# Performance work log

Measured on AMD Instinct MI355X. Metric: run time of the kernel, lower is better.

## Reference

```python
import jax, jax.numpy as jnp
import numpy as np

BATCH, LENGTH, IN, STATE, OUT = 8, 4096, 512, 256, 512


def setup_inputs() -> dict:
    key = jax.random.key(0)
    k1, k2, k3, k4, k5 = jax.random.split(key, 5)
    u = jax.random.normal(k1, (BATCH, LENGTH, IN), dtype=jnp.float32)
    x0 = jax.random.normal(k2, (BATCH, STATE), dtype=jnp.float32)
    A = 0.9999 * (2.0 * jax.random.uniform(k3, (STATE,), dtype=jnp.float32) - 1.0)
    B = jax.random.normal(k4, (IN, STATE), dtype=jnp.float32) / (STATE + IN) ** 0.5
    C = jax.random.normal(k5, (STATE, OUT), dtype=jnp.float32) / STATE ** 0.5
    return {"u": u, "x0": x0, "A": A, "B": B, "C": C}


def reference(u, x0, A, B, C):
    L = u.shape[1]
    # A_powers[t, n] = A[n] ** t, shape [L, state]
    A_powers = jnp.power(A[None, :], jnp.arange(L, dtype=u.dtype)[:, None])
    uB = u @ B  # [batch, L, state]
    # FFT convolution; inputs are real so rfft/irfft gives same result as
    # real(ifft(fft*fft)) in the original.
    T = 2 ** int(np.ceil(np.log2(2 * L - 1)))
    Af = jnp.fft.rfft(A_powers, n=T, axis=0)  # [T/2+1, state]
    Uf = jnp.fft.rfft(uB, n=T, axis=1)        # [batch, T/2+1, state]
    x = jnp.fft.irfft(Af[None, :, :] * Uf, n=T, axis=1)[:, :L]  # [batch, L, state]
    # initial-state contribution: A * A_powers * x0
    x = x + A[None, None, :] * A_powers[None, :, :] * x0[:, None, :]
    y = x @ C  # [batch, L, out]
    return (y, x[:, -1])
```

## Files before the change

### kernel.cpp

```cpp
#include <hip/hip_runtime.h>

#define BATCH   8
#define LENGTH  4096
#define IN_DIM  512
#define STATE   256
#define OUT_DIM 512
#define NC      64
#define LC      64

typedef __attribute__((ext_vector_type(8))) short bf16x8;
typedef __attribute__((ext_vector_type(4))) float f32x4;

union FragU { bf16x8 v; unsigned u[4]; };

__device__ __forceinline__ unsigned short bf16_rne(float v) {
    unsigned u = __builtin_bit_cast(unsigned, v);
    unsigned r = (u + 0x7FFFu + ((u >> 16) & 1u)) >> 16;
    return (unsigned short)r;
}
__device__ __forceinline__ float bf16_f(unsigned short h) {
    unsigned u = ((unsigned)h) << 16;
    return __builtin_bit_cast(float, u);
}

__global__ __launch_bounds__(256) void split_T_kernel(
    const float* __restrict__ in, unsigned short* __restrict__ hi,
    unsigned short* __restrict__ lo, int kbits, int Nsrc)
{
    int id = blockIdx.x * 256 + threadIdx.x;
    int k = id & ((1 << kbits) - 1);
    int n = id >> kbits;
    float v = in[(size_t)k * Nsrc + n];
    unsigned short h = bf16_rne(v);
    hi[id] = h;
    lo[id] = bf16_rne(v - bf16_f(h));
}

__global__ __launch_bounds__(512, 4) void gemm_dbuf(
    const float* __restrict__ Af, const unsigned short* __restrict__ Bthi,
    const unsigned short* __restrict__ Btlo, float* __restrict__ Cc,
    int N_, int K)
{
    __shared__ unsigned short lds[2 * 16384];

    const int tid  = threadIdx.x;
    const int wave = tid >> 6;
    const int lane = tid & 63;
    const int n0 = blockIdx.x * 128;
    const int m0 = blockIdx.y * 128;

    const char* gp[4];
    int ldsoff[4], gstep[4];
    #pragma unroll
    for (int t = 0; t < 4; ++t) {
        int gi = wave * 4 + t;
        if (gi < 16) {
            int p = gi * 64 + lane;
            int row = p >> 3, s = p & 7;
            int l = s ^ (row & 7);
            gp[t] = (const char*)(Af + (size_t)(m0 + row) * K + l * 4);
            gstep[t] = 32 * 4;
            ldsoff[t] = gi * 512;
        } else {
            int q2 = (gi - 16) >> 3;
            int pi = gi & 7;
            int p = pi * 64 + lane;
            int row = p >> 2, s = p & 3;
            int l = s ^ ((row >> 1) & 3);
            const unsigned short* base = q2 ? Btlo : Bthi;
            gp[t] = (const char*)(base + (size_t)(n0 + row) * K + l * 8);
            gstep[t] = 32 * 2;
            ldsoff[t] = 8192 + q2 * 4096 + pi * 512;
        }
    }

    const int r = lane & 15, q = lane >> 4;
    const int wm = (wave >> 2) * 64, wn = (wave & 3) * 32;

    int aoff[4][2], boff[2];
    #pragma unroll
    for (int i = 0; i < 4; ++i) {
        int row = wm + i * 16 + r;
        #pragma unroll
        for (int h = 0; h < 2; ++h)
            aoff[i][h] = row * 64 + ((2 * q + h) ^ (row & 7)) * 8;
    }
    #pragma unroll
    for (int j = 0; j < 2; ++j) {
        int row = wn + j * 16 + r;
        boff[j] = row * 32 + (q ^ ((row >> 1) & 3)) * 8;
    }

    f32x4 acc[4][2];
    #pragma unroll
    for (int i = 0; i < 4; ++i)
        #pragma unroll
        for (int j = 0; j < 2; ++j)
            acc[i][j] = (f32x4){0.f, 0.f, 0.f, 0.f};

    #pragma unroll
    for (int t = 0; t < 4; ++t) {
        __builtin_amdgcn_global_load_lds(
            (const __attribute__((address_space(1))) unsigned*)(gp[t]),
            (__attribute__((address_space(3))) unsigned*)(&lds[ldsoff[t]]),
            16, 0, 0);
        gp[t] += gstep[t];
    }

    const int nit = K >> 5;
    for (int it = 0; it < nit; ++it) {
        asm volatile("" ::: "memory");
        __builtin_amdgcn_s_barrier();
        asm volatile("" ::: "memory");
        if (it + 1 < nit) {
            const int bb = ((it + 1) & 1) * 16384;
            #pragma unroll
            for (int t = 0; t < 4; ++t) {
                __builtin_amdgcn_global_load_lds(
                    (const __attribute__((address_space(1))) unsigned*)(gp[t]),
                    (__attribute__((address_space(3))) unsigned*)(&lds[bb + ldsoff[t]]),
                    16, 0, 0);
                gp[t] += gstep[t];
            }
            __builtin_amdgcn_s_waitcnt(0x0F74);
        } else {
            __builtin_amdgcn_s_waitcnt(0x0F70);
        }
        asm volatile("" ::: "memory");
        __builtin_amdgcn_s_barrier();
        asm volatile("" ::: "memory");

        const unsigned short* buf = &lds[(it & 1) * 16384];

        FragU ahi[4], alo[4];
        #pragma unroll
        for (int i = 0; i < 4; ++i) {
            #pragma unroll
            for (int h = 0; h < 2; ++h) {
                float4 f = *(const float4*)(buf + aoff[i][h]);
                unsigned bx = __builtin_bit_cast(unsigned, f.x);
                unsigned by = __builtin_bit_cast(unsigned, f.y);
                unsigned bz = __builtin_bit_cast(unsigned, f.z);
                unsigned bw = __builtin_bit_cast(unsigned, f.w);
                ahi[i].u[h * 2]     = __builtin_amdgcn_perm(by, bx, 0x07060302);
                ahi[i].u[h * 2 + 1] = __builtin_amdgcn_perm(bw, bz, 0x07060302);
                float lx = f.x - __builtin_bit_cast(float, bx & 0xFFFF0000u);
                float ly = f.y - __builtin_bit_cast(float, by & 0xFFFF0000u);
                float lz = f.z - __builtin_bit_cast(float, bz & 0xFFFF0000u);
                float lw = f.w - __builtin_bit_cast(float, bw & 0xFFFF0000u);
                alo[i].u[h * 2]     = __builtin_amdgcn_perm(
                    __builtin_bit_cast(unsigned, ly), __builtin_bit_cast(unsigned, lx), 0x07060302);
                alo[i].u[h * 2 + 1] = __builtin_amdgcn_perm(
                    __builtin_bit_cast(unsigned, lw), __builtin_bit_cast(unsigned, lz), 0x07060302);
            }
        }
        FragU bhi[2], blo[2];
        #pragma unroll
        for (int j = 0; j < 2; ++j) {
            bhi[j].v = *(const bf16x8*)(buf +  8192 + boff[j]);
            blo[j].v = *(const bf16x8*)(buf + 12288 + boff[j]);
        }
        #pragma unroll
        for (int i = 0; i < 4; ++i)
            #pragma unroll
            for (int j = 0; j < 2; ++j) {
                acc[i][j] = __builtin_amdgcn_mfma_f32_16x16x32_bf16(ahi[i].v, bhi[j].v, acc[i][j], 0, 0, 0);
                acc[i][j] = __builtin_amdgcn_mfma_f32_16x16x32_bf16(alo[i].v, bhi[j].v, acc[i][j], 0, 0, 0);
                acc[i][j] = __builtin_amdgcn_mfma_f32_16x16x32_bf16(ahi[i].v, blo[j].v, acc[i][j], 0, 0, 0);
            }
    }

    #pragma unroll
    for (int i = 0; i < 4; ++i) {
        #pragma unroll
        for (int reg = 0; reg < 4; ++reg) {
            int mg = m0 + wm + i * 16 + q * 4 + reg;
            float* dst = Cc + (size_t)mg * N_ + n0 + wn + r;
            dst[0]  = acc[i][0][reg];
            dst[16] = acc[i][1][reg];
        }
    }
}

__global__ __launch_bounds__(256) void scan_carry(
    const float* __restrict__ uB, const float* __restrict__ A,
    float* __restrict__ carry)
{
    const int b = blockIdx.x;
    const int c = blockIdx.y;
    const int n = threadIdx.x;
    const float a = A[n];
    const float* p = uB + ((size_t)b * LENGTH + (size_t)c * LC) * STATE + n;
    float s = 0.f;
    #pragma unroll 8
    for (int j = 0; j < LC; ++j) s = a * s + p[(size_t)j * STATE];
    carry[((size_t)b * NC + c) * STATE + n] = s;
}

__global__ __launch_bounds__(256) void scan_apply(
    const float* __restrict__ uB, const float* __restrict__ A,
    const float* __restrict__ carry, const float* __restrict__ x0,
    float* __restrict__ x, float* __restrict__ x_last)
{
    const int b = blockIdx.x;
    const int c = blockIdx.y;
    const int n = threadIdx.x;
    const float a = A[n];
    float a2 = a * a, a4 = a2 * a2, a8 = a4 * a4, a16 = a8 * a8, a32 = a16 * a16;
    const float aLC = a32 * a32;

    float s = x0[(size_t)b * STATE + n];
    for (int d = 0; d < c; ++d)
        s = aLC * s + carry[((size_t)b * NC + d) * STATE + n];

    const size_t base = ((size_t)b * LENGTH + (size_t)c * LC) * STATE + n;
    const float* p = uB + base;
    float* qx = x + base;
    #pragma unroll 8
    for (int j = 0; j < LC; ++j) {
        s = a * s + p[(size_t)j * STATE];
        qx[(size_t)j * STATE] = s;
    }
    if (c == NC - 1) x_last[(size_t)b * STATE + n] = s;
}

extern "C" void kernel_launch(void* const* d_in, const int* in_sizes, int n_in,
                              void* d_out, int out_size, void* d_ws, size_t ws_size,
                              hipStream_t stream)
{
    const float* u  = (const float*)d_in[0];
    const float* x0 = (const float*)d_in[1];
    const float* A  = (const float*)d_in[2];
    const float* B  = (const float*)d_in[3];
    const float* C  = (const float*)d_in[4];

    const size_t MB = 1024 * 1024;
    char* ws = (char*)d_ws;

    float* x     = (float*)(ws);
    float* carry = (float*)(ws + 32 * MB);
    unsigned short* Bt_hi = (unsigned short*)(ws + 33 * MB);
    unsigned short* Bt_lo = (unsigned short*)(ws + 33 * MB + 256 * 1024);
    unsigned short* Ct_hi = (unsigned short*)(ws + 33 * MB + 512 * 1024);
    unsigned short* Ct_lo = (unsigned short*)(ws + 33 * MB + 768 * 1024);

    float* y      = (float*)d_out;
    float* x_last = y + (size_t)BATCH * LENGTH * OUT_DIM;
    float* uB     = (float*)((char*)d_out + 32 * MB);

    const int M = BATCH * LENGTH;

    split_T_kernel<<<dim3((IN_DIM * STATE) / 256), dim3(256), 0, stream>>>(B, Bt_hi, Bt_lo, 9, STATE);
    split_T_kernel<<<dim3((STATE * OUT_DIM) / 256), dim3(256), 0, stream>>>(C, Ct_hi, Ct_lo, 8, OUT_DIM);

    gemm_dbuf<<<dim3(STATE / 128, M / 128), dim3(512), 0, stream>>>(
        u, Bt_hi, Bt_lo, uB, STATE, IN_DIM);

    scan_carry<<<dim3(BATCH, NC), dim3(256), 0, stream>>>(uB, A, carry);
    scan_apply<<<dim3(BATCH, NC), dim3(256), 0, stream>>>(uB, A, carry, x0, x, x_last);

    gemm_dbuf<<<dim3(OUT_DIM / 128, M / 128), dim3(512), 0, stream>>>(
        x, Ct_hi, Ct_lo, y, OUT_DIM, STATE);
}
```

Baseline: 207.7 us.

## Emit bf16 hi/lo planes from scan and add presplit GEMM for output projection

The scan now writes the state as two bf16 planes (hi and lo) instead of fp32. A new GEMM kernel loads those pre-split planes straight into LDS, so the second GEMM skips the per-iteration fp32 split work. The two weight-split kernels are merged into one launch, and the first GEMM's wave tiling changes from 64x32 to 32x64 per wave. The lo plane comes from truncating the residual rather than rounding it, which slightly changes numerics.

```diff
diff --git a/kernel.cpp b/kernel.cpp
--- a/kernel.cpp
+++ b/kernel.cpp
@@ -23,17 +23,26 @@
     return __builtin_bit_cast(float, u);
 }
 
-__global__ __launch_bounds__(256) void split_T_kernel(
-    const float* __restrict__ in, unsigned short* __restrict__ hi,
-    unsigned short* __restrict__ lo, int kbits, int Nsrc)
+__global__ __launch_bounds__(256) void split_weights(
+    const float* __restrict__ B, const float* __restrict__ C,
+    unsigned short* __restrict__ Bhi, unsigned short* __restrict__ Blo,
+    unsigned short* __restrict__ Chi, unsigned short* __restrict__ Clo)
 {
     int id = blockIdx.x * 256 + threadIdx.x;
-    int k = id & ((1 << kbits) - 1);
-    int n = id >> kbits;
-    float v = in[(size_t)k * Nsrc + n];
-    unsigned short h = bf16_rne(v);
-    hi[id] = h;
-    lo[id] = bf16_rne(v - bf16_f(h));
+    if (id < IN_DIM * STATE) {
+        int k = id & (IN_DIM - 1), n = id >> 9;
+        float v = B[(size_t)k * STATE + n];
+        unsigned short h = bf16_rne(v);
+        Bhi[id] = h;
+        Blo[id] = bf16_rne(v - bf16_f(h));
+    } else {
+        int id2 = id - IN_DIM * STATE;
+        int k = id2 & (STATE - 1), n = id2 >> 8;
+        float v = C[(size_t)k * OUT_DIM + n];
+        unsigned short h = bf16_rne(v);
+        Chi[id2] = h;
+        Clo[id2] = bf16_rne(v - bf16_f(h));
+    }
 }
 
 __global__ __launch_bounds__(512, 4) void gemm_dbuf(
@@ -75,27 +84,27 @@
     }
 
     const int r = lane & 15, q = lane >> 4;
-    const int wm = (wave >> 2) * 64, wn = (wave & 3) * 32;
-
-    int aoff[4][2], boff[2];
-    #pragma unroll
-    for (int i = 0; i < 4; ++i) {
+    const int wm = (wave >> 1) * 32, wn = (wave & 1) * 64;
+
+    int aoff[2][2], boff[4];
+    #pragma unroll
+    for (int i = 0; i < 2; ++i) {
         int row = wm + i * 16 + r;
         #pragma unroll
         for (int h = 0; h < 2; ++h)
             aoff[i][h] = row * 64 + ((2 * q + h) ^ (row & 7)) * 8;
     }
     #pragma unroll
-    for (int j = 0; j < 2; ++j) {
+    for (int j = 0; j < 4; ++j) {
         int row = wn + j * 16 + r;
         boff[j] = row * 32 + (q ^ ((row >> 1) & 3)) * 8;
     }
 
-    f32x4 acc[4][2];
-    #pragma unroll
-    for (int i = 0; i < 4; ++i)
-        #pragma unroll
-        for (int j = 0; j < 2; ++j)
+    f32x4 acc[2][4];
+    #pragma unroll
+    for (int i = 0; i < 2; ++i)
+        #pragma unroll
+        for (int j = 0; j < 4; ++j)
             acc[i][j] = (f32x4){0.f, 0.f, 0.f, 0.f};
 
     #pragma unroll
@@ -132,9 +141,9 @@
 
         const unsigned short* buf = &lds[(it & 1) * 16384];
 
-        FragU ahi[4], alo[4];
-        #pragma unroll
-        for (int i = 0; i < 4; ++i) {
+        FragU ahi[2], alo[2];
+        #pragma unroll
+        for (int i = 0; i < 2; ++i) {
             #pragma unroll
             for (int h = 0; h < 2; ++h) {
                 float4 f = *(const float4*)(buf + aoff[i][h]);
@@ -154,6 +163,128 @@
                     __builtin_bit_cast(unsigned, lw), __builtin_bit_cast(unsigned, lz), 0x07060302);
             }
         }
+        FragU bhi[4], blo[4];
+        #pragma unroll
+        for (int j = 0; j < 4; ++j) {
+            bhi[j].v = *(const bf16x8*)(buf +  8192 + boff[j]);
+            blo[j].v = *(const bf16x8*)(buf + 12288 + boff[j]);
+        }
+        #pragma unroll
+        for (int i = 0; i < 2; ++i)
+            #pragma unroll
+            for (int j = 0; j < 4; ++j) {
+                acc[i][j] = __builtin_amdgcn_mfma_f32_16x16x32_bf16(ahi[i].v, bhi[j].v, acc[i][j], 0, 0, 0);
+                acc[i][j] = __builtin_amdgcn_mfma_f32_16x16x32_bf16(alo[i].v, bhi[j].v, acc[i][j], 0, 0, 0);
+                acc[i][j] = __builtin_amdgcn_mfma_f32_16x16x32_bf16(ahi[i].v, blo[j].v, acc[i][j], 0, 0, 0);
+            }
+    }
+
+    #pragma unroll
+    for (int i = 0; i < 2; ++i) {
+        #pragma unroll
+        for (int reg = 0; reg < 4; ++reg) {
+            int mg = m0 + wm + i * 16 + q * 4 + reg;
+            float* dst = Cc + (size_t)mg * N_ + n0 + wn + r;
+            dst[0]  = acc[i][0][reg];
+            dst[16] = acc[i][1][reg];
+            dst[32] = acc[i][2][reg];
+            dst[48] = acc[i][3][reg];
+        }
+    }
+}
+
+__global__ __launch_bounds__(512, 4) void gemm_presplit(
+    const unsigned short* __restrict__ Athi, const unsigned short* __restrict__ Atlo,
+    const unsigned short* __restrict__ Bthi, const unsigned short* __restrict__ Btlo,
+    float* __restrict__ Cc, int N_, int K)
+{
+    __shared__ unsigned short lds[2 * 16384];
+
+    const int tid  = threadIdx.x;
+    const int wave = tid >> 6;
+    const int lane = tid & 63;
+    const int n0 = blockIdx.x * 128;
+    const int m0 = blockIdx.y * 128;
+
+    const char* gp[4];
+    int ldsoff[4];
+    #pragma unroll
+    for (int t = 0; t < 4; ++t) {
+        int gi = wave * 4 + t;
+        int plane = gi >> 3;
+        int pi = gi & 7;
+        int p = pi * 64 + lane;
+        int row = p >> 2, s = p & 3;
+        int l = s ^ ((row >> 1) & 3);
+        const unsigned short* base =
+            (plane == 0) ? Athi : (plane == 1) ? Atlo : (plane == 2) ? Bthi : Btlo;
+        int r0 = (plane < 2) ? m0 : n0;
+        gp[t] = (const char*)(base + (size_t)(r0 + row) * K + l * 8);
+        ldsoff[t] = plane * 4096 + pi * 512;
+    }
+
+    const int r = lane & 15, q = lane >> 4;
+    const int wm = (wave >> 2) * 64, wn = (wave & 3) * 32;
+
+    int aoff[4], boff[2];
+    #pragma unroll
+    for (int i = 0; i < 4; ++i) {
+        int row = wm + i * 16 + r;
+        aoff[i] = row * 32 + (q ^ ((row >> 1) & 3)) * 8;
+    }
+    #pragma unroll
+    for (int j = 0; j < 2; ++j) {
+        int row = wn + j * 16 + r;
+        boff[j] = row * 32 + (q ^ ((row >> 1) & 3)) * 8;
+    }
+
+    f32x4 acc[4][2];
+    #pragma unroll
+    for (int i = 0; i < 4; ++i)
+        #pragma unroll
+        for (int j = 0; j < 2; ++j)
+            acc[i][j] = (f32x4){0.f, 0.f, 0.f, 0.f};
+
+    #pragma unroll
+    for (int t = 0; t < 4; ++t) {
+        __builtin_amdgcn_global_load_lds(
+            (const __attribute__((address_space(1))) unsigned*)(gp[t]),
+            (__attribute__((address_space(3))) unsigned*)(&lds[ldsoff[t]]),
+            16, 0, 0);
+        gp[t] += 64;
+    }
+
+    const int nit = K >> 5;
+    for (int it = 0; it < nit; ++it) {
+        asm volatile("" ::: "memory");
+        __builtin_amdgcn_s_barrier();
+        asm volatile("" ::: "memory");
+        if (it + 1 < nit) {
+            const int bb = ((it + 1) & 1) * 16384;
+            #pragma unroll
+            for (int t = 0; t < 4; ++t) {
+                __builtin_amdgcn_global_load_lds(
+                    (const __attribute__((address_space(1))) unsigned*)(gp[t]),
+                    (__attribute__((address_space(3))) unsigned*)(&lds[bb + ldsoff[t]]),
+                    16, 0, 0);
+                gp[t] += 64;
+            }
+            __builtin_amdgcn_s_waitcnt(0x0F74);
+        } else {
+            __builtin_amdgcn_s_waitcnt(0x0F70);
+        }
+        asm volatile("" ::: "memory");
+        __builtin_amdgcn_s_barrier();
+        asm volatile("" ::: "memory");
+
+        const unsigned short* buf = &lds[(it & 1) * 16384];
+
+        FragU ahi[4], alo[4];
+        #pragma unroll
+        for (int i = 0; i < 4; ++i) {
+            ahi[i].v = *(const bf16x8*)(buf +        aoff[i]);
+            alo[i].v = *(const bf16x8*)(buf + 4096 + aoff[i]);
+        }
         FragU bhi[2], blo[2];
         #pragma unroll
         for (int j = 0; j < 2; ++j) {
@@ -200,7 +331,8 @@
 __global__ __launch_bounds__(256) void scan_apply(
     const float* __restrict__ uB, const float* __restrict__ A,
     const float* __restrict__ carry, const float* __restrict__ x0,
-    float* __restrict__ x, float* __restrict__ x_last)
+    unsigned short* __restrict__ xhi, unsigned short* __restrict__ xlo,
+    float* __restrict__ x_last)
 {
     const int b = blockIdx.x;
     const int c = blockIdx.y;
@@ -215,11 +347,15 @@
 
     const size_t base = ((size_t)b * LENGTH + (size_t)c * LC) * STATE + n;
     const float* p = uB + base;
-    float* qx = x + base;
+    unsigned short* qh = xhi + base;
+    unsigned short* ql = xlo + base;
     #pragma unroll 8
     for (int j = 0; j < LC; ++j) {
         s = a * s + p[(size_t)j * STATE];
-        qx[(size_t)j * STATE] = s;
+        unsigned u = __builtin_bit_cast(unsigned, s);
+        qh[(size_t)j * STATE] = (unsigned short)(u >> 16);
+        float lo = s - __builtin_bit_cast(float, u & 0xFFFF0000u);
+        ql[(size_t)j * STATE] = (unsigned short)(__builtin_bit_cast(unsigned, lo) >> 16);
     }
     if (c == NC - 1) x_last[(size_t)b * STATE + n] = s;
 }
@@ -237,7 +373,8 @@
     const size_t MB = 1024 * 1024;
     char* ws = (char*)d_ws;
 
-    float* x     = (float*)(ws);
+    unsigned short* xhi = (unsigned short*)(ws);
+    unsigned short* xlo = (unsigned short*)(ws + 16 * MB);
     float* carry = (float*)(ws + 32 * MB);
     unsigned short* Bt_hi = (unsigned short*)(ws + 33 * MB);
     unsigned short* Bt_lo = (unsigned short*)(ws + 33 * MB + 256 * 1024);
@@ -250,15 +387,15 @@
 
     const int M = BATCH * LENGTH;
 
-    split_T_kernel<<<dim3((IN_DIM * STATE) / 256), dim3(256), 0, stream>>>(B, Bt_hi, Bt_lo, 9, STATE);
-    split_T_kernel<<<dim3((STATE * OUT_DIM) / 256), dim3(256), 0, stream>>>(C, Ct_hi, Ct_lo, 8, OUT_DIM);
+    split_weights<<<dim3((IN_DIM * STATE + STATE * OUT_DIM) / 256), dim3(256), 0, stream>>>(
+        B, C, Bt_hi, Bt_lo, Ct_hi, Ct_lo);
 
     gemm_dbuf<<<dim3(STATE / 128, M / 128), dim3(512), 0, stream>>>(
         u, Bt_hi, Bt_lo, uB, STATE, IN_DIM);
 
     scan_carry<<<dim3(BATCH, NC), dim3(256), 0, stream>>>(uB, A, carry);
-    scan_apply<<<dim3(BATCH, NC), dim3(256), 0, stream>>>(uB, A, carry, x0, x, x_last);
-
-    gemm_dbuf<<<dim3(OUT_DIM / 128, M / 128), dim3(512), 0, stream>>>(
-        x, Ct_hi, Ct_lo, y, OUT_DIM, STATE);
-}
+    scan_apply<<<dim3(BATCH, NC), dim3(256), 0, stream>>>(uB, A, carry, x0, xhi, xlo, x_last);
+
+    gemm_presplit<<<dim3(OUT_DIM / 128, M / 128), dim3(512), 0, stream>>>(
+        xhi, xlo, Ct_hi, Ct_lo, y, OUT_DIM, STATE);
+}
```

Result: faster. 200.0 us (-3.7%).
